# Optimization experiments

Measured on AMD Instinct MI355X. Metric: run time of the kernel, lower is better.

## Reference

```python
import jax, jax.numpy as jnp
import numpy as np
import math

SQRT_2_OVER_PI = 0.7978845608028654  # sqrt(2/pi)
EPS = 1e-12  # F.normalize eps


def _gelu_tanh(x):
    return 0.5 * x * (1.0 + jnp.tanh(SQRT_2_OVER_PI * (x + 0.044715 * x * x * x)))


def _l2norm(v, axis=-1):
    n = jnp.sqrt(jnp.sum(v * v, axis=axis, keepdims=True))
    return v / jnp.maximum(n, EPS)


def setup_inputs() -> dict:
    key = jax.random.key(0)
    k1, k2 = jax.random.split(key)
    B, T, D = 8, 2048, 2048
    N_TRAIN = 16
    x = jax.random.normal(k1, (B, T, D), dtype=jnp.float32)
    # ring buffer stores L2-normalized token-mean vectors
    buf = jax.random.normal(k2, (N_TRAIN, D), dtype=jnp.float32)
    train_buf = _l2norm(buf, axis=-1)
    train_mask = jnp.ones((N_TRAIN,), dtype=bool)  # steady state: buffer full
    log_tau = jnp.asarray(math.log(2.0), dtype=jnp.float32)
    log_blend_train = jnp.asarray(math.log(0.3 / 0.7), dtype=jnp.float32)
    return {
        "x": x,
        "train_buf": train_buf,
        "train_mask": train_mask,
        "log_tau": log_tau,
        "log_blend_train": log_blend_train,
    }


def reference(x, train_buf, train_mask, log_tau, log_blend_train):
    B, T, D = x.shape
    tau = jnp.exp(log_tau)
    alpha = jax.nn.sigmoid(log_blend_train)
    # elementwise tanh-GELU
    y = _gelu_tanh(x)  # (B, T, D)
    # gate path uses detached activations (y.detach() in torch)
    y_flat = jax.lax.stop_gradient(y.reshape(B * T, D))
    y_n = _l2norm(y_flat, axis=-1)            # (BT, D)
    buf_n = _l2norm(train_buf, axis=-1)       # (N, D)
    sims = y_n @ buf_n.T                      # (BT, N) skinny matmul
    sims = jnp.where(train_mask[None, :], sims, jnp.asarray(-1.0, sims.dtype))
    max_sim = jnp.max(sims, axis=-1)          # (BT,)
    gate = 1.0 - alpha + alpha * jnp.exp(-tau * max_sim)  # (BT,)
    # training mode: test-buffer gate is all ones -> combined gate == train gate
    return y * gate.reshape(B, T, 1)
```

## Files before the change

kernel.cpp:

```cpp
#include <hip/hip_runtime.h>

#define LOG2E 1.4426950408889634f

constexpr int D     = 2048;
constexpr int NB    = 16;
constexpr int TPB   = 256;
constexpr int NROWS = 16384;
constexpr int RPB   = 4;
constexpr int NBLK  = NROWS / RPB;
constexpr int NKT   = 16;

typedef short bf16x8 __attribute__((ext_vector_type(8)));
typedef float f32x4  __attribute__((ext_vector_type(4)));
typedef float vfloat4 __attribute__((ext_vector_type(4)));

__device__ __forceinline__ float gelu_tanh_f(float x) {
    const float C = 0.7978845608028654f;
    const float K = 0.044715f;
    float x2 = x * x;
    float p  = __builtin_fmaf(K, x2, 1.0f);
    float z  = C * x * p;
    float e  = __builtin_amdgcn_exp2f(z * (2.0f * LOG2E));
    float th = 1.0f - 2.0f * __builtin_amdgcn_rcpf(e + 1.0f);
    float hx = 0.5f * x;
    return __builtin_fmaf(hx, th, hx);
}

__device__ __forceinline__ unsigned bpack(float a, float b) {
    unsigned ua = __builtin_bit_cast(unsigned, a);
    unsigned ub = __builtin_bit_cast(unsigned, b);
    ua += 0x7FFFu + ((ua >> 16) & 1u);
    ub += 0x7FFFu + ((ub >> 16) & 1u);
    return (ua >> 16) | (ub & 0xFFFF0000u);
}
__device__ __forceinline__ float blo(unsigned w) {
    return __builtin_bit_cast(float, w << 16);
}
__device__ __forceinline__ float bhi(unsigned w) {
    return __builtin_bit_cast(float, w & 0xFFFF0000u);
}

__global__ void __launch_bounds__(512) bfrag_kernel(
    const float* __restrict__ buf, unsigned* __restrict__ bfrag)
{
    const int id = blockIdx.x * 512 + threadIdx.x;
    const int n  = (id >> 2) & 15;
    const int k  = ((id >> 8) << 5) + (((id >> 6) & 3) << 3) + ((id & 3) << 1);
    const float* p = buf + n * D + k;
    bfrag[id] = bpack(p[0], p[1]);
}

__global__ void __launch_bounds__(TPB) gelu_gate_kernel(
    const float* __restrict__ x,
    const unsigned* __restrict__ bfrag,
    const int* __restrict__ mask_i,
    const unsigned char* __restrict__ mask_b,
    const float* __restrict__ p_log_tau,
    const float* __restrict__ p_log_blend,
    float* __restrict__ out)
{
    __shared__ unsigned ldsY[RPB * D / 2];
    __shared__ f32x4    ldsAcc[4][16];
    __shared__ float    ldsS2[4][4];

    const int t    = threadIdx.x;
    const int lane = t & 63;
    const int wk   = t >> 6;

    const float tau   = __builtin_amdgcn_exp2f(p_log_tau[0] * LOG2E);
    const float lbt   = p_log_blend[0];
    const float alpha = __builtin_amdgcn_rcpf(1.0f + __builtin_amdgcn_exp2f(-lbt * LOG2E));

    unsigned mbits = 0;
#pragma unroll
    for (int k = 0; k < NB; ++k) {
        bool mk = (mask_i[k] != 0) || (mask_b[k] != 0);
        mbits |= (mk ? 1u : 0u) << k;
    }

    const int row0 = blockIdx.x * RPB;
    const float4* x4   = reinterpret_cast<const float4*>(x);
    vfloat4*      out4 = reinterpret_cast<vfloat4*>(out);
    char* ldsYb = reinterpret_cast<char*>(ldsY);

    float4 v[RPB][2];
#pragma unroll
    for (int j = 0; j < RPB; ++j) {
        v[j][0] = x4[(size_t)(row0 + j) * (D / 4) + 2 * t];
        v[j][1] = x4[(size_t)(row0 + j) * (D / 4) + 2 * t + 1];
    }
    uint4 ypk[RPB];
    float p2[RPB];
#pragma unroll
    for (int j = 0; j < RPB; ++j) {
        float y0 = gelu_tanh_f(v[j][0].x), y1 = gelu_tanh_f(v[j][0].y);
        float y2 = gelu_tanh_f(v[j][0].z), y3 = gelu_tanh_f(v[j][0].w);
        float y4 = gelu_tanh_f(v[j][1].x), y5 = gelu_tanh_f(v[j][1].y);
        float y6 = gelu_tanh_f(v[j][1].z), y7 = gelu_tanh_f(v[j][1].w);
        float s = y0 * y0;
        s = __builtin_fmaf(y1, y1, s); s = __builtin_fmaf(y2, y2, s);
        s = __builtin_fmaf(y3, y3, s); s = __builtin_fmaf(y4, y4, s);
        s = __builtin_fmaf(y5, y5, s); s = __builtin_fmaf(y6, y6, s);
        s = __builtin_fmaf(y7, y7, s);
        p2[j] = s;
        uint4 w;
        w.x = bpack(y0, y1); w.y = bpack(y2, y3);
        w.z = bpack(y4, y5); w.w = bpack(y6, y7);
        ypk[j] = w;
        const int byte = j * 4096 + ((16 * t) ^ (j << 6));
        *reinterpret_cast<uint4*>(ldsYb + byte) = w;
    }
    {
        const bool b5 = lane & 32, b4 = lane & 16;
        float e0 = (b5 ? p2[2] : p2[0]) + __shfl_xor(b5 ? p2[0] : p2[2], 32, 64);
        float e1 = (b5 ? p2[3] : p2[1]) + __shfl_xor(b5 ? p2[1] : p2[3], 32, 64);
        float f  = (b4 ? e1 : e0) + __shfl_xor(b4 ? e0 : e1, 16, 64);
        f += __shfl_xor(f, 8, 64);
        f += __shfl_xor(f, 4, 64);
        f += __shfl_xor(f, 2, 64);
        f += __shfl_xor(f, 1, 64);
        if ((lane & 15) == 0) ldsS2[wk][lane >> 4] = f;
    }
    __syncthreads();

    const int m    = lane & 15;
    const int mr   = m & 3;
    const int kgrp = lane >> 4;
    const char* aRow = ldsYb + mr * 4096;
    const int swz    = mr << 6;
    const unsigned* Bb = bfrag + wk * (NKT * 256) + lane * 4;

    f32x4 acc = {0.f, 0.f, 0.f, 0.f};
#pragma unroll
    for (int kt = 0; kt < NKT; ++kt) {
        const int off = wk * 1024 + kt * 64 + kgrp * 16;
        const uint4 af = *reinterpret_cast<const uint4*>(aRow + (off ^ swz));
        const uint4 bq = *reinterpret_cast<const uint4*>(Bb + kt * 256);
        acc = __builtin_amdgcn_mfma_f32_16x16x32_bf16(
            __builtin_bit_cast(bf16x8, af), __builtin_bit_cast(bf16x8, bq),
            acc, 0, 0, 0);
    }

    if (lane < 16) ldsAcc[wk][lane] = acc;
    __syncthreads();

    const int n = lane & 15;
    f32x4 dt = ldsAcc[0][n];
#pragma unroll
    for (int w = 1; w < 4; ++w) dt += ldsAcc[w][n];

    float gate[4];
#pragma unroll
    for (int j = 0; j < 4; ++j) {
        const float s2t = ldsS2[0][j] + ldsS2[1][j] + ldsS2[2][j] + ldsS2[3][j];
        const float inv = __builtin_amdgcn_rcpf(fmaxf(__builtin_sqrtf(s2t), 1e-12f));
        float s = dt[j] * inv;
        if (!((mbits >> n) & 1u)) s = -1.0f;
        s = fmaxf(s, __shfl_xor(s, 1, 64));
        s = fmaxf(s, __shfl_xor(s, 2, 64));
        s = fmaxf(s, __shfl_xor(s, 4, 64));
        s = fmaxf(s, __shfl_xor(s, 8, 64));
        gate[j] = __builtin_fmaf(alpha, __builtin_amdgcn_exp2f(-tau * s * LOG2E),
                                 1.0f - alpha);
    }

#pragma unroll
    for (int j = 0; j < RPB; ++j) {
        const uint4 w = ypk[j];
        const float gj = gate[j];
        vfloat4 o1, o2;
        o1.x = blo(w.x) * gj; o1.y = bhi(w.x) * gj;
        o1.z = blo(w.y) * gj; o1.w = bhi(w.y) * gj;
        o2.x = blo(w.z) * gj; o2.y = bhi(w.z) * gj;
        o2.z = blo(w.w) * gj; o2.w = bhi(w.w) * gj;
        __builtin_nontemporal_store(o1, &out4[(size_t)(row0 + j) * (D / 4) + 2 * t]);
        __builtin_nontemporal_store(o2, &out4[(size_t)(row0 + j) * (D / 4) + 2 * t + 1]);
    }
}

extern "C" void kernel_launch(void* const* d_in, const int* in_sizes, int n_in,
                              void* d_out, int out_size, void* d_ws, size_t ws_size,
                              hipStream_t stream) {
    const float*         x      = (const float*)d_in[0];
    const float*         buf    = (const float*)d_in[1];
    const int*           mask_i = (const int*)d_in[2];
    const unsigned char* mask_b = (const unsigned char*)d_in[2];
    const float*         lt     = (const float*)d_in[3];
    const float*         lb     = (const float*)d_in[4];
    float*               out    = (float*)d_out;
    unsigned*            bfrag  = (unsigned*)d_ws;

    bfrag_kernel<<<32, 512, 0, stream>>>(buf, bfrag);
    gelu_gate_kernel<<<NBLK, TPB, 0, stream>>>(x, bfrag, mask_i, mask_b, lt, lb, out);
}
```

Before: 61.10 us.

## Process two row tiles per block, prefetching next tile's input during compute

Each block now handles two 4-row tiles in sequence. The global loads for the second tile are issued before the first tile's MFMA and gate work, so their latency overlaps that compute. Barriers are replaced by a custom lgkmcnt wait plus s_barrier so outstanding global loads are not waited on. Packed activations are re-read from LDS rather than kept in registers, and output stores switch from nontemporal to normal. The costs are halving the grid to 2048 blocks and adding an extra barrier between tiles.

Result: no change. 60.14 us (-1.6%).

```diff
diff --git a/kernel.cpp b/kernel.cpp
--- a/kernel.cpp
+++ b/kernel.cpp
@@ -7,12 +7,12 @@
 constexpr int TPB   = 256;
 constexpr int NROWS = 16384;
 constexpr int RPB   = 4;
-constexpr int NBLK  = NROWS / RPB;
+constexpr int TILES = 2;
+constexpr int NBLK  = NROWS / (RPB * TILES);
 constexpr int NKT   = 16;
 
 typedef short bf16x8 __attribute__((ext_vector_type(8)));
 typedef float f32x4  __attribute__((ext_vector_type(4)));
-typedef float vfloat4 __attribute__((ext_vector_type(4)));
 
 __device__ __forceinline__ float gelu_tanh_f(float x) {
     const float C = 0.7978845608028654f;
@@ -38,6 +38,11 @@
 }
 __device__ __forceinline__ float bhi(unsigned w) {
     return __builtin_bit_cast(float, w & 0xFFFF0000u);
+}
+
+__device__ __forceinline__ void lds_barrier() {
+    asm volatile("s_waitcnt lgkmcnt(0)" ::: "memory");
+    __builtin_amdgcn_s_barrier();
 }
 
 __global__ void __launch_bounds__(512) bfrag_kernel(
@@ -78,50 +83,10 @@
         mbits |= (mk ? 1u : 0u) << k;
     }
 
-    const int row0 = blockIdx.x * RPB;
+    const int rowB = blockIdx.x * (RPB * TILES);
     const float4* x4   = reinterpret_cast<const float4*>(x);
-    vfloat4*      out4 = reinterpret_cast<vfloat4*>(out);
+    float4*       out4 = reinterpret_cast<float4*>(out);
     char* ldsYb = reinterpret_cast<char*>(ldsY);
-
-    float4 v[RPB][2];
-#pragma unroll
-    for (int j = 0; j < RPB; ++j) {
-        v[j][0] = x4[(size_t)(row0 + j) * (D / 4) + 2 * t];
-        v[j][1] = x4[(size_t)(row0 + j) * (D / 4) + 2 * t + 1];
-    }
-    uint4 ypk[RPB];
-    float p2[RPB];
-#pragma unroll
-    for (int j = 0; j < RPB; ++j) {
-        float y0 = gelu_tanh_f(v[j][0].x), y1 = gelu_tanh_f(v[j][0].y);
-        float y2 = gelu_tanh_f(v[j][0].z), y3 = gelu_tanh_f(v[j][0].w);
-        float y4 = gelu_tanh_f(v[j][1].x), y5 = gelu_tanh_f(v[j][1].y);
-        float y6 = gelu_tanh_f(v[j][1].z), y7 = gelu_tanh_f(v[j][1].w);
-        float s = y0 * y0;
-        s = __builtin_fmaf(y1, y1, s); s = __builtin_fmaf(y2, y2, s);
-        s = __builtin_fmaf(y3, y3, s); s = __builtin_fmaf(y4, y4, s);
-        s = __builtin_fmaf(y5, y5, s); s = __builtin_fmaf(y6, y6, s);
-        s = __builtin_fmaf(y7, y7, s);
-        p2[j] = s;
-        uint4 w;
-        w.x = bpack(y0, y1); w.y = bpack(y2, y3);
-        w.z = bpack(y4, y5); w.w = bpack(y6, y7);
-        ypk[j] = w;
-        const int byte = j * 4096 + ((16 * t) ^ (j << 6));
-        *reinterpret_cast<uint4*>(ldsYb + byte) = w;
-    }
-    {
-        const bool b5 = lane & 32, b4 = lane & 16;
-        float e0 = (b5 ? p2[2] : p2[0]) + __shfl_xor(b5 ? p2[0] : p2[2], 32, 64);
-        float e1 = (b5 ? p2[3] : p2[1]) + __shfl_xor(b5 ? p2[1] : p2[3], 32, 64);
-        float f  = (b4 ? e1 : e0) + __shfl_xor(b4 ? e0 : e1, 16, 64);
-        f += __shfl_xor(f, 8, 64);
-        f += __shfl_xor(f, 4, 64);
-        f += __shfl_xor(f, 2, 64);
-        f += __shfl_xor(f, 1, 64);
-        if ((lane & 15) == 0) ldsS2[wk][lane >> 4] = f;
-    }
-    __syncthreads();
 
     const int m    = lane & 15;
     const int mr   = m & 3;
@@ -130,51 +95,107 @@
     const int swz    = mr << 6;
     const unsigned* Bb = bfrag + wk * (NKT * 256) + lane * 4;
 
-    f32x4 acc = {0.f, 0.f, 0.f, 0.f};
-#pragma unroll
-    for (int kt = 0; kt < NKT; ++kt) {
-        const int off = wk * 1024 + kt * 64 + kgrp * 16;
-        const uint4 af = *reinterpret_cast<const uint4*>(aRow + (off ^ swz));
-        const uint4 bq = *reinterpret_cast<const uint4*>(Bb + kt * 256);
-        acc = __builtin_amdgcn_mfma_f32_16x16x32_bf16(
-            __builtin_bit_cast(bf16x8, af), __builtin_bit_cast(bf16x8, bq),
-            acc, 0, 0, 0);
+    float4 v[RPB][2];
+#pragma unroll
+    for (int j = 0; j < RPB; ++j) {
+        v[j][0] = x4[(size_t)(rowB + j) * (D / 4) + 2 * t];
+        v[j][1] = x4[(size_t)(rowB + j) * (D / 4) + 2 * t + 1];
     }
 
-    if (lane < 16) ldsAcc[wk][lane] = acc;
-    __syncthreads();
-
-    const int n = lane & 15;
-    f32x4 dt = ldsAcc[0][n];
-#pragma unroll
-    for (int w = 1; w < 4; ++w) dt += ldsAcc[w][n];
-
-    float gate[4];
-#pragma unroll
-    for (int j = 0; j < 4; ++j) {
-        const float s2t = ldsS2[0][j] + ldsS2[1][j] + ldsS2[2][j] + ldsS2[3][j];
-        const float inv = __builtin_amdgcn_rcpf(fmaxf(__builtin_sqrtf(s2t), 1e-12f));
-        float s = dt[j] * inv;
-        if (!((mbits >> n) & 1u)) s = -1.0f;
-        s = fmaxf(s, __shfl_xor(s, 1, 64));
-        s = fmaxf(s, __shfl_xor(s, 2, 64));
-        s = fmaxf(s, __shfl_xor(s, 4, 64));
-        s = fmaxf(s, __shfl_xor(s, 8, 64));
-        gate[j] = __builtin_fmaf(alpha, __builtin_amdgcn_exp2f(-tau * s * LOG2E),
-                                 1.0f - alpha);
-    }
-
-#pragma unroll
-    for (int j = 0; j < RPB; ++j) {
-        const uint4 w = ypk[j];
-        const float gj = gate[j];
-        vfloat4 o1, o2;
-        o1.x = blo(w.x) * gj; o1.y = bhi(w.x) * gj;
-        o1.z = blo(w.y) * gj; o1.w = bhi(w.y) * gj;
-        o2.x = blo(w.z) * gj; o2.y = bhi(w.z) * gj;
-        o2.z = blo(w.w) * gj; o2.w = bhi(w.w) * gj;
-        __builtin_nontemporal_store(o1, &out4[(size_t)(row0 + j) * (D / 4) + 2 * t]);
-        __builtin_nontemporal_store(o2, &out4[(size_t)(row0 + j) * (D / 4) + 2 * t + 1]);
+#pragma unroll
+    for (int tl = 0; tl < TILES; ++tl) {
+        const int r0 = rowB + tl * RPB;
+
+        float p2[RPB];
+#pragma unroll
+        for (int j = 0; j < RPB; ++j) {
+            float y0 = gelu_tanh_f(v[j][0].x), y1 = gelu_tanh_f(v[j][0].y);
+            float y2 = gelu_tanh_f(v[j][0].z), y3 = gelu_tanh_f(v[j][0].w);
+            float y4 = gelu_tanh_f(v[j][1].x), y5 = gelu_tanh_f(v[j][1].y);
+            float y6 = gelu_tanh_f(v[j][1].z), y7 = gelu_tanh_f(v[j][1].w);
+            float s = y0 * y0;
+            s = __builtin_fmaf(y1, y1, s); s = __builtin_fmaf(y2, y2, s);
+            s = __builtin_fmaf(y3, y3, s); s = __builtin_fmaf(y4, y4, s);
+            s = __builtin_fmaf(y5, y5, s); s = __builtin_fmaf(y6, y6, s);
+            s = __builtin_fmaf(y7, y7, s);
+            p2[j] = s;
+            uint4 w;
+            w.x = bpack(y0, y1); w.y = bpack(y2, y3);
+            w.z = bpack(y4, y5); w.w = bpack(y6, y7);
+            *reinterpret_cast<uint4*>(ldsYb + j * 4096 + ((16 * t) ^ (j << 6))) = w;
+        }
+        {
+            const bool b5 = lane & 32, b4 = lane & 16;
+            float e0 = (b5 ? p2[2] : p2[0]) + __shfl_xor(b5 ? p2[0] : p2[2], 32, 64);
+            float e1 = (b5 ? p2[3] : p2[1]) + __shfl_xor(b5 ? p2[1] : p2[3], 32, 64);
+            float f  = (b4 ? e1 : e0) + __shfl_xor(b4 ? e0 : e1, 16, 64);
+            f += __shfl_xor(f, 8, 64);
+            f += __shfl_xor(f, 4, 64);
+            f += __shfl_xor(f, 2, 64);
+            f += __shfl_xor(f, 1, 64);
+            if ((lane & 15) == 0) ldsS2[wk][lane >> 4] = f;
+        }
+
+        if (tl + 1 < TILES) {
+#pragma unroll
+            for (int j = 0; j < RPB; ++j) {
+                v[j][0] = x4[(size_t)(r0 + RPB + j) * (D / 4) + 2 * t];
+                v[j][1] = x4[(size_t)(r0 + RPB + j) * (D / 4) + 2 * t + 1];
+            }
+        }
+
+        lds_barrier();
+
+        f32x4 acc = {0.f, 0.f, 0.f, 0.f};
+#pragma unroll
+        for (int kt = 0; kt < NKT; ++kt) {
+            const int off = wk * 1024 + kt * 64 + kgrp * 16;
+            const uint4 af = *reinterpret_cast<const uint4*>(aRow + (off ^ swz));
+            const uint4 bq = *reinterpret_cast<const uint4*>(Bb + kt * 256);
+            acc = __builtin_amdgcn_mfma_f32_16x16x32_bf16(
+                __builtin_bit_cast(bf16x8, af), __builtin_bit_cast(bf16x8, bq),
+                acc, 0, 0, 0);
+        }
+        if (lane < 16) ldsAcc[wk][lane] = acc;
+
+        lds_barrier();
+
+        const int n = lane & 15;
+        f32x4 dt = ldsAcc[0][n];
+#pragma unroll
+        for (int w = 1; w < 4; ++w) dt += ldsAcc[w][n];
+
+        float gate[4];
+#pragma unroll
+        for (int j = 0; j < 4; ++j) {
+            const float s2t = ldsS2[0][j] + ldsS2[1][j] + ldsS2[2][j] + ldsS2[3][j];
+            const float inv = __builtin_amdgcn_rcpf(fmaxf(__builtin_sqrtf(s2t), 1e-12f));
+            float s = dt[j] * inv;
+            if (!((mbits >> n) & 1u)) s = -1.0f;
+            s = fmaxf(s, __shfl_xor(s, 1, 64));
+            s = fmaxf(s, __shfl_xor(s, 2, 64));
+            s = fmaxf(s, __shfl_xor(s, 4, 64));
+            s = fmaxf(s, __shfl_xor(s, 8, 64));
+            gate[j] = __builtin_fmaf(alpha, __builtin_amdgcn_exp2f(-tau * s * LOG2E),
+                                     1.0f - alpha);
+        }
+
+#pragma unroll
+        for (int j = 0; j < RPB; ++j) {
+            const uint4 w = *reinterpret_cast<const uint4*>(
+                ldsYb + j * 4096 + ((16 * t) ^ (j << 6)));
+            const float gj = gate[j];
+            float4 o1, o2;
+            o1.x = blo(w.x) * gj; o1.y = bhi(w.x) * gj;
+            o1.z = blo(w.y) * gj; o1.w = bhi(w.y) * gj;
+            o2.x = blo(w.z) * gj; o2.y = bhi(w.z) * gj;
+            o2.z = blo(w.w) * gj; o2.w = bhi(w.w) * gj;
+            out4[(size_t)(r0 + j) * (D / 4) + 2 * t]     = o1;
+            out4[(size_t)(r0 + j) * (D / 4) + 2 * t + 1] = o2;
+        }
+
+        if (tl + 1 < TILES)
+            lds_barrier();
     }
 }
 
```
